# Kernel tuning notes

Measured on AMD Instinct MI355X. Metric: run time of the kernel, lower is better.

Reference implementation:

```python
import jax, jax.numpy as jnp
import numpy as np

D_MODEL = 1024
N_HEAD = 16
D_HEAD = D_MODEL // N_HEAD
B, S = 4, 2048


def setup_inputs() -> dict:
    key = jax.random.key(0)
    ks = jax.random.split(key, 9)
    s = 1.0 / np.sqrt(D_MODEL)
    inp = {"x": jax.random.normal(ks[0], (B, S, D_MODEL), dtype=jnp.float32)}
    for i, name in enumerate(["q", "k", "v", "o"]):
        inp[f"W{name}"] = jax.random.uniform(ks[1 + 2 * i], (D_MODEL, D_MODEL), jnp.float32, -s, s)
        inp[f"b{name}"] = jax.random.uniform(ks[2 + 2 * i], (D_MODEL,), jnp.float32, -s, s)
    return inp


def reference(x, Wq, bq, Wk, bk, Wv, bv, Wo, bo):
    b, sq, _ = x.shape
    skv = sq
    # projections (torch Linear: x @ W^T + b), reshape to (b, h, s, d)
    def proj(W, bias):
        return (x @ W.T + bias).reshape(b, sq, N_HEAD, D_HEAD).transpose(0, 2, 1, 3)
    q, k, v = proj(Wq, bq), proj(Wk, bk), proj(Wv, bv)
    scale = np.sqrt(D_HEAD).astype(np.float32)
    scores = jnp.einsum("bhqd,bhkd->bhqk", q, k) / scale
    causal_mask = jnp.triu(jnp.ones((sq, skv), dtype=bool), k=1)
    scores = jnp.where(causal_mask, -jnp.inf, scores)
    attn = jax.nn.softmax(scores, axis=-1)
    o = jnp.einsum("bhqk,bhkd->bhqd", attn, v)  # (b, h, sq, d_head)
    o = o.transpose(0, 2, 1, 3).reshape(b, sq, D_MODEL)
    return o @ Wo.T + bo
```

## Files before the change

kernel.cpp:

```cpp
#include <hip/hip_runtime.h>
#include <hip/hip_bf16.h>
#include <math.h>

#define S_LEN 2048
#define DMODEL 1024
#define NHEAD 16
#define DHEAD 64
#define BATCH 4
#define MROWS (BATCH * S_LEN)

typedef unsigned short u16;
typedef __attribute__((ext_vector_type(4))) unsigned short u16x4;
typedef __attribute__((ext_vector_type(8))) unsigned short u16x8;
typedef __attribute__((ext_vector_type(2))) unsigned u32x2;
typedef __attribute__((ext_vector_type(4))) unsigned u32x4;
typedef __attribute__((ext_vector_type(8))) short bf16x8;
typedef __attribute__((ext_vector_type(4))) float f32x4;

__device__ __forceinline__ u16 f2bf(float f) {
  unsigned u = __float_as_uint(f);
  u += 0x7fff + ((u >> 16) & 1);
  return (u16)(u >> 16);
}

__device__ __forceinline__ unsigned pkbf2(float lo, float hi) {
  __hip_bfloat162 h = __float22bfloat162_rn(float2{lo, hi});
  unsigned r;
  __builtin_memcpy(&r, &h, 4);
  return r;
}

__device__ __forceinline__ float exp2v(float x) {
  float r;
  asm("v_exp_f32 %0, %1" : "=v"(r) : "v"(x));
  return r;
}

__device__ __forceinline__ f32x4 mfma16(bf16x8 a, bf16x8 b, f32x4 c) {
  return __builtin_amdgcn_mfma_f32_16x16x32_bf16(a, b, c, 0, 0, 0);
}

__global__ __launch_bounds__(256) void castall(
    const float* __restrict__ x,
    const float* __restrict__ w0, const float* __restrict__ w1,
    const float* __restrict__ w2, const float* __restrict__ w3,
    u16* __restrict__ ox,
    u16* __restrict__ o0, u16* __restrict__ o1,
    u16* __restrict__ o2, u16* __restrict__ o3) {
  const int blk = blockIdx.x;
  const float* in;
  u16* out;
  int base;
  if (blk < 4096)      { in = x;  out = ox; base = blk; }
  else if (blk < 4608) { in = w0; out = o0; base = blk - 4096; }
  else if (blk < 5120) { in = w1; out = o1; base = blk - 4608; }
  else if (blk < 5632) { in = w2; out = o2; base = blk - 5120; }
  else                 { in = w3; out = o3; base = blk - 5632; }
  const int i = (base * 256 + threadIdx.x) * 8;
  f32x4 v0 = *(const f32x4*)(in + i);
  f32x4 v1 = *(const f32x4*)(in + i + 4);
  u16x8 o;
#pragma unroll
  for (int j = 0; j < 4; ++j) { o[j] = f2bf(v0[j]); o[4 + j] = f2bf(v1[j]); }
  *(u16x8*)(out + i) = o;
}

__global__ __launch_bounds__(256) void gemm_qkv(
    const u16* __restrict__ Xb,
    const u16* __restrict__ W0, const u16* __restrict__ W1, const u16* __restrict__ W2,
    const float* __restrict__ b0, const float* __restrict__ b1, const float* __restrict__ b2,
    u16* __restrict__ O0, u16* __restrict__ O1, u16* __restrict__ O2) {
  __shared__ u16 As[128 * 64];
  __shared__ u16 Bs[128 * 64];
  const int flat = blockIdx.x;
  const int xcd = flat & 7, idx = flat >> 3;
  const int msub = idx & 7;
  const int nz = idx >> 3;
  const int ymt = xcd * 8 + msub;
  const int xnt = nz & 7;
  const int z = nz >> 3;
  const u16* Wm = z == 0 ? W0 : (z == 1 ? W1 : W2);
  const float* bias = z == 0 ? b0 : (z == 1 ? b1 : b2);
  u16* Out = z == 0 ? O0 : (z == 1 ? O1 : O2);
  const float qs = (z == 0) ? 0.18033688011112042f : 1.0f;
  const int tid = threadIdx.x;
  const int lane = tid & 63, g = lane >> 4, c = lane & 15;
  const int wave = tid >> 6;
  const int wm = wave >> 1, wn = wave & 1;
  const int bm0 = ymt * 128, bn0 = xnt * 128;

  int srow[4], scol[4];
#pragma unroll
  for (int cc = 0; cc < 4; ++cc) {
    const int ci = cc * 256 + tid;
    srow[cc] = ci >> 3;
    scol[cc] = ((ci & 7) ^ (srow[cc] & 7)) << 3;
  }

  f32x4 acc[4][4];
#pragma unroll
  for (int m = 0; m < 4; ++m)
#pragma unroll
    for (int n = 0; n < 4; ++n) acc[m][n] = (f32x4){0.f, 0.f, 0.f, 0.f};

  u32x4 ar0, ar1, ar2, ar3, br0, br1, br2, br3;
#define GLOAD(k0_) do {                                                        \
    ar0 = *(const u32x4*)(Xb + (size_t)(bm0 + srow[0]) * DMODEL + (k0_) + scol[0]); \
    br0 = *(const u32x4*)(Wm + (size_t)(bn0 + srow[0]) * DMODEL + (k0_) + scol[0]); \
    ar1 = *(const u32x4*)(Xb + (size_t)(bm0 + srow[1]) * DMODEL + (k0_) + scol[1]); \
    br1 = *(const u32x4*)(Wm + (size_t)(bn0 + srow[1]) * DMODEL + (k0_) + scol[1]); \
    ar2 = *(const u32x4*)(Xb + (size_t)(bm0 + srow[2]) * DMODEL + (k0_) + scol[2]); \
    br2 = *(const u32x4*)(Wm + (size_t)(bn0 + srow[2]) * DMODEL + (k0_) + scol[2]); \
    ar3 = *(const u32x4*)(Xb + (size_t)(bm0 + srow[3]) * DMODEL + (k0_) + scol[3]); \
    br3 = *(const u32x4*)(Wm + (size_t)(bn0 + srow[3]) * DMODEL + (k0_) + scol[3]); \
  } while (0)

  GLOAD(0);
  for (int k0 = 0; k0 < DMODEL; k0 += 64) {
    __syncthreads();
    *(u32x4*)((char*)As + (0 * 256 + tid) * 16) = ar0;
    *(u32x4*)((char*)Bs + (0 * 256 + tid) * 16) = br0;
    *(u32x4*)((char*)As + (1 * 256 + tid) * 16) = ar1;
    *(u32x4*)((char*)Bs + (1 * 256 + tid) * 16) = br1;
    *(u32x4*)((char*)As + (2 * 256 + tid) * 16) = ar2;
    *(u32x4*)((char*)Bs + (2 * 256 + tid) * 16) = br2;
    *(u32x4*)((char*)As + (3 * 256 + tid) * 16) = ar3;
    *(u32x4*)((char*)Bs + (3 * 256 + tid) * 16) = br3;
    __syncthreads();
    if (k0 + 64 < DMODEL) GLOAD(k0 + 64);
#pragma unroll
    for (int ks = 0; ks < 2; ++ks) {
      bf16x8 af[4], bfr[4];
#pragma unroll
      for (int m = 0; m < 4; ++m) {
        const int arow = wm * 64 + m * 16 + c;
        af[m] = *(const bf16x8*)((const char*)As + arow * 128 +
                                 (((ks * 4 + g) ^ (arow & 7)) << 4));
      }
#pragma unroll
      for (int n = 0; n < 4; ++n) {
        const int brow = wn * 64 + n * 16 + c;
        bfr[n] = *(const bf16x8*)((const char*)Bs + brow * 128 +
                                  (((ks * 4 + g) ^ (brow & 7)) << 4));
      }
#pragma unroll
      for (int m = 0; m < 4; ++m)
#pragma unroll
        for (int n = 0; n < 4; ++n)
          acc[m][n] = mfma16(af[m], bfr[n], acc[m][n]);
    }
  }
#undef GLOAD
  if (z < 2) {
#pragma unroll
    for (int n = 0; n < 4; ++n) {
      const int coln = bn0 + wn * 64 + n * 16 + c;
      const float bn_ = bias[coln];
      const int h = coln >> 6, d = coln & 63;
#pragma unroll
      for (int m = 0; m < 4; ++m) {
#pragma unroll
        for (int r = 0; r < 4; ++r) {
          const int rowm = bm0 + wm * 64 + m * 16 + g * 4 + r;
          const int b_ = rowm >> 11, s_ = rowm & 2047;
          Out[(((size_t)(b_ * NHEAD + h) * S_LEN + s_) << 6) + d] =
              f2bf((acc[m][n][r] + bn_) * qs);
        }
      }
    }
  } else {
#pragma unroll
    for (int n = 0; n < 4; ++n) {
      const int coln = bn0 + wn * 64 + n * 16 + c;
      const float bn_ = bias[coln];
      const int h = coln >> 6, d = coln & 63;
#pragma unroll
      for (int m = 0; m < 4; ++m) {
        const int row0 = bm0 + wm * 64 + m * 16 + g * 4;
        const int b_ = row0 >> 11, s_ = row0 & 2047;
        u16x4 pk;
#pragma unroll
        for (int r = 0; r < 4; ++r) pk[r] = f2bf(acc[m][n][r] + bn_);
        *(u16x4*)(Out + ((size_t)(b_ * NHEAD + h) * DHEAD + d) * S_LEN + s_) = pk;
      }
    }
  }
}

__global__ __launch_bounds__(256) void gemm_out(
    const u16* __restrict__ Ab, const u16* __restrict__ Wm,
    const float* __restrict__ bias, float* __restrict__ Out) {
  __shared__ u16 As[128 * 64];
  __shared__ u16 Bs[128 * 64];
  const int flat = blockIdx.x;
  const int xcd = flat & 7, idx = flat >> 3;
  const int ymt = xcd * 8 + (idx & 7);
  const int xnt = idx >> 3;
  const int tid = threadIdx.x;
  const int lane = tid & 63, g = lane >> 4, c = lane & 15;
  const int wave = tid >> 6;
  const int wm = wave >> 1, wn = wave & 1;
  const int bm0 = ymt * 128, bn0 = xnt * 128;

  int srow[4], scol[4];
#pragma unroll
  for (int cc = 0; cc < 4; ++cc) {
    const int ci = cc * 256 + tid;
    srow[cc] = ci >> 3;
    scol[cc] = ((ci & 7) ^ (srow[cc] & 7)) << 3;
  }

  f32x4 acc[4][4];
#pragma unroll
  for (int m = 0; m < 4; ++m)
#pragma unroll
    for (int n = 0; n < 4; ++n) acc[m][n] = (f32x4){0.f, 0.f, 0.f, 0.f};

  u32x4 ar0, ar1, ar2, ar3, br0, br1, br2, br3;
#define GLOAD(k0_) do {                                                        \
    ar0 = *(const u32x4*)(Ab + (size_t)(bm0 + srow[0]) * DMODEL + (k0_) + scol[0]); \
    br0 = *(const u32x4*)(Wm + (size_t)(bn0 + srow[0]) * DMODEL + (k0_) + scol[0]); \
    ar1 = *(const u32x4*)(Ab + (size_t)(bm0 + srow[1]) * DMODEL + (k0_) + scol[1]); \
    br1 = *(const u32x4*)(Wm + (size_t)(bn0 + srow[1]) * DMODEL + (k0_) + scol[1]); \
    ar2 = *(const u32x4*)(Ab + (size_t)(bm0 + srow[2]) * DMODEL + (k0_) + scol[2]); \
    br2 = *(const u32x4*)(Wm + (size_t)(bn0 + srow[2]) * DMODEL + (k0_) + scol[2]); \
    ar3 = *(const u32x4*)(Ab + (size_t)(bm0 + srow[3]) * DMODEL + (k0_) + scol[3]); \
    br3 = *(const u32x4*)(Wm + (size_t)(bn0 + srow[3]) * DMODEL + (k0_) + scol[3]); \
  } while (0)

  GLOAD(0);
  for (int k0 = 0; k0 < DMODEL; k0 += 64) {
    __syncthreads();
    *(u32x4*)((char*)As + (0 * 256 + tid) * 16) = ar0;
    *(u32x4*)((char*)Bs + (0 * 256 + tid) * 16) = br0;
    *(u32x4*)((char*)As + (1 * 256 + tid) * 16) = ar1;
    *(u32x4*)((char*)Bs + (1 * 256 + tid) * 16) = br1;
    *(u32x4*)((char*)As + (2 * 256 + tid) * 16) = ar2;
    *(u32x4*)((char*)Bs + (2 * 256 + tid) * 16) = br2;
    *(u32x4*)((char*)As + (3 * 256 + tid) * 16) = ar3;
    *(u32x4*)((char*)Bs + (3 * 256 + tid) * 16) = br3;
    __syncthreads();
    if (k0 + 64 < DMODEL) GLOAD(k0 + 64);
#pragma unroll
    for (int ks = 0; ks < 2; ++ks) {
      bf16x8 af[4], bfr[4];
#pragma unroll
      for (int m = 0; m < 4; ++m) {
        const int arow = wm * 64 + m * 16 + c;
        af[m] = *(const bf16x8*)((const char*)As + arow * 128 +
                                 (((ks * 4 + g) ^ (arow & 7)) << 4));
      }
#pragma unroll
      for (int n = 0; n < 4; ++n) {
        const int brow = wn * 64 + n * 16 + c;
        bfr[n] = *(const bf16x8*)((const char*)Bs + brow * 128 +
                                  (((ks * 4 + g) ^ (brow & 7)) << 4));
      }
#pragma unroll
      for (int m = 0; m < 4; ++m)
#pragma unroll
        for (int n = 0; n < 4; ++n)
          acc[m][n] = mfma16(af[m], bfr[n], acc[m][n]);
    }
  }
#undef GLOAD
#pragma unroll
  for (int n = 0; n < 4; ++n) {
    const int coln = bn0 + wn * 64 + n * 16 + c;
    const float bn_ = bias[coln];
#pragma unroll
    for (int m = 0; m < 4; ++m) {
#pragma unroll
      for (int r = 0; r < 4; ++r) {
        const int rowm = bm0 + wm * 64 + m * 16 + g * 4 + r;
        Out[(size_t)rowm * DMODEL + coln] = acc[m][n][r] + bn_;
      }
    }
  }
}

__global__ __launch_bounds__(512) void attn_fwd(const u16* __restrict__ Qb,
                                                const u16* __restrict__ Kb,
                                                const u16* __restrict__ VTb,
                                                u16* __restrict__ AOb) {
  __shared__ u16 Kt[64 * 64];
  __shared__ u16 Vt[64 * 64];
  __shared__ unsigned Pl[8][16 * 36];
  const int tid = threadIdx.x;
  const int w = tid >> 6, lane = tid & 63, g = lane >> 4, c = lane & 15;
  const int flat = blockIdx.x;
  const int xcd = flat & 7, idx = flat >> 3;
  const int qt16 = 15 - (idx >> 3);
  const int bh = xcd * 8 + (idx & 7);
  const size_t base = (size_t)bh * (S_LEN * DHEAD);
  const int b_ = bh >> 4, h = bh & 15;

  const int row0_ = tid >> 3, colg0 = (tid & 7) ^ (row0_ & 7);

  const int qb = qt16 * 128;
  const int q = qb + w * 16 + c;
  const bf16x8 qf0 = *(const bf16x8*)(Qb + base + (size_t)q * 64 + g * 8);
  const bf16x8 qf1 = *(const bf16x8*)(Qb + base + (size_t)q * 64 + 32 + g * 8);

  bf16x8 ones;
#pragma unroll
  for (int j = 0; j < 8; ++j) ones[j] = (short)0x3F80;

  f32x4 oacc[4];
  f32x4 lacc = (f32x4){0.f, 0.f, 0.f, 0.f};
#pragma unroll
  for (int dt = 0; dt < 4; ++dt) oacc[dt] = (f32x4){0.f, 0.f, 0.f, 0.f};
  float m = -30000.f;

  u32x4 kreg0, vreg0;
#define STAGE_LOAD(kt_) do {                                                  \
    const int kv0_ = (kt_) * 64;                                              \
    kreg0 = *(const u32x4*)(Kb + base + (size_t)(kv0_ + row0_) * 64 + colg0 * 8); \
    vreg0 = *(const u32x4*)(VTb + base + (size_t)row0_ * S_LEN + kv0_ + colg0 * 8); \
  } while (0)

  const int nt = 2 * qt16 + 2;
  STAGE_LOAD(0);
  for (int kt = 0; kt < nt; ++kt) {
    const int kv0 = kt * 64;
    __syncthreads();
    *(u32x4*)((char*)Kt + tid * 16) = kreg0;
    *(u32x4*)((char*)Vt + tid * 16) = vreg0;
    __syncthreads();
    if (kt + 1 < nt) STAGE_LOAD(kt + 1);

    f32x4 s[4];
#pragma unroll
    for (int t = 0; t < 4; ++t) {
      const int krow = t * 16 + c;
      const char* kbase = (const char*)Kt + krow * 128;
      bf16x8 kf0 = *(const bf16x8*)(kbase + ((g ^ (krow & 7)) * 16));
      bf16x8 kf1 = *(const bf16x8*)(kbase + (((4 + g) ^ (krow & 7)) * 16));
      f32x4 zacc = (f32x4){0.f, 0.f, 0.f, 0.f};
      zacc = mfma16(kf0, qf0, zacc);
      zacc = mfma16(kf1, qf1, zacc);
      s[t] = zacc;
    }
    if (kt >= nt - 2) {
#pragma unroll
      for (int t = 0; t < 4; ++t)
#pragma unroll
        for (int r = 0; r < 4; ++r)
          if (kv0 + t * 16 + 4 * g + r > q) s[t][r] = -30000.f;
    }
    const float a0 = fmaxf(fmaxf(s[0][0], s[0][1]), s[0][2]);
    const float a1 = fmaxf(fmaxf(s[0][3], s[1][0]), s[1][1]);
    const float a2 = fmaxf(fmaxf(s[1][2], s[1][3]), s[2][0]);
    const float a3 = fmaxf(fmaxf(s[2][1], s[2][2]), s[2][3]);
    const float a4 = fmaxf(fmaxf(s[3][0], s[3][1]), s[3][2]);
    float pm = fmaxf(fmaxf(fmaxf(a0, a1), a2), fmaxf(fmaxf(a3, a4), s[3][3]));
    pm = fmaxf(pm, __shfl_xor(pm, 16));
    pm = fmaxf(pm, __shfl_xor(pm, 32));
    if (__any(pm > m + 8.0f)) {
      const float mn = fmaxf(m, pm);
      const float sc = exp2v(m - mn);
      lacc *= sc;
#pragma unroll
      for (int dt = 0; dt < 4; ++dt) oacc[dt] *= sc;
      m = mn;
    }
#pragma unroll
    for (int t = 0; t < 4; ++t) {
      const float p0 = exp2v(s[t][0] - m), p1 = exp2v(s[t][1] - m);
      const float p2 = exp2v(s[t][2] - m), p3 = exp2v(s[t][3] - m);
      u32x2 pk2;
      pk2[0] = pkbf2(p0, p1);
      pk2[1] = pkbf2(p2, p3);
      *(u32x2*)&Pl[w][c * 36 + t * 8 + g * 2] = pk2;
    }

#pragma unroll
    for (int kk = 0; kk < 2; ++kk) {
      const bf16x8 pb = *(const bf16x8*)&Pl[w][c * 36 + kk * 16 + g * 4];
      lacc = mfma16(ones, pb, lacc);
#pragma unroll
      for (int dt = 0; dt < 4; ++dt) {
        const int vrow = dt * 16 + c;
        const bf16x8 vf = *(const bf16x8*)((const char*)Vt + vrow * 128 +
                                           (((kk * 4 + g) ^ (vrow & 7)) * 16));
        oacc[dt] = mfma16(vf, pb, oacc[dt]);
      }
    }
  }
#undef STAGE_LOAD
  const float inv = 1.0f / lacc[0];
  const size_t rowbase = ((size_t)(b_ * S_LEN + q) * DMODEL) + h * 64;
#pragma unroll
  for (int dt = 0; dt < 4; ++dt) {
    u16x4 pk4;
#pragma unroll
    for (int r = 0; r < 4; ++r) pk4[r] = f2bf(oacc[dt][r] * inv);
    *(u16x4*)(AOb + rowbase + dt * 16 + 4 * g) = pk4;
  }
}

extern "C" void kernel_launch(void* const* d_in, const int* in_sizes, int n_in,
                              void* d_out, int out_size, void* d_ws, size_t ws_size,
                              hipStream_t stream) {
  const float* x  = (const float*)d_in[0];
  const float* Wq = (const float*)d_in[1];
  const float* bq = (const float*)d_in[2];
  const float* Wk = (const float*)d_in[3];
  const float* bk = (const float*)d_in[4];
  const float* Wv = (const float*)d_in[5];
  const float* bv = (const float*)d_in[6];
  const float* Wo = (const float*)d_in[7];
  const float* bo = (const float*)d_in[8];
  float* out = (float*)d_out;
  char* ws = (char*)d_ws;

  const size_t MB = 1024 * 1024;
  u16* xb  = (u16*)(ws);
  u16* Wqb = (u16*)(ws + 16 * MB);
  u16* Wkb = (u16*)(ws + 18 * MB);
  u16* Wvb = (u16*)(ws + 20 * MB);
  u16* Wob = (u16*)(ws + 22 * MB);
  u16* Qb  = (u16*)(ws + 24 * MB);
  u16* Kb  = (u16*)(ws + 40 * MB);
  u16* VTb = (u16*)(ws + 56 * MB);
  u16* AOb = (u16*)(ws + 72 * MB);

  castall<<<6144, 256, 0, stream>>>(x, Wq, Wk, Wv, Wo, xb, Wqb, Wkb, Wvb, Wob);

  gemm_qkv<<<1536, 256, 0, stream>>>(
      xb, Wqb, Wkb, Wvb, bq, bk, bv, Qb, Kb, VTb);

  attn_fwd<<<1024, 512, 0, stream>>>(Qb, Kb, VTb, AOb);

  gemm_out<<<512, 256, 0, stream>>>(AOb, Wob, bo, out);
}
```

Measured before the change: 158.3 us.

## Enlarge QKV GEMM tile to 256x128 with 512-thread blocks

Doubles the M dimension of the QKV projection GEMM block tile to 256 rows and uses 8 waves per block, so each staged B (weight) tile is reused across twice as many rows. Grid is halved to 768 blocks and LDS for A doubles. The aim is to cut global and LDS traffic per FLOP, at the cost of fewer blocks, higher LDS use per block and possibly lower occupancy.

```diff
diff --git a/kernel.cpp b/kernel.cpp
--- a/kernel.cpp
+++ b/kernel.cpp
@@ -65,18 +65,18 @@
   *(u16x8*)(out + i) = o;
 }
 
-__global__ __launch_bounds__(256) void gemm_qkv(
+__global__ __launch_bounds__(512) void gemm_qkv(
     const u16* __restrict__ Xb,
     const u16* __restrict__ W0, const u16* __restrict__ W1, const u16* __restrict__ W2,
     const float* __restrict__ b0, const float* __restrict__ b1, const float* __restrict__ b2,
     u16* __restrict__ O0, u16* __restrict__ O1, u16* __restrict__ O2) {
-  __shared__ u16 As[128 * 64];
+  __shared__ u16 As[256 * 64];
   __shared__ u16 Bs[128 * 64];
   const int flat = blockIdx.x;
   const int xcd = flat & 7, idx = flat >> 3;
-  const int msub = idx & 7;
-  const int nz = idx >> 3;
-  const int ymt = xcd * 8 + msub;
+  const int msub = idx & 3;
+  const int nz = idx >> 2;
+  const int ymt = xcd * 4 + msub;
   const int xnt = nz & 7;
   const int z = nz >> 3;
   const u16* Wm = z == 0 ? W0 : (z == 1 ? W1 : W2);
@@ -87,14 +87,20 @@
   const int lane = tid & 63, g = lane >> 4, c = lane & 15;
   const int wave = tid >> 6;
   const int wm = wave >> 1, wn = wave & 1;
-  const int bm0 = ymt * 128, bn0 = xnt * 128;
-
-  int srow[4], scol[4];
+  const int bm0 = ymt * 256, bn0 = xnt * 128;
+
+  int arowS[4], acolS[4], browS[2], bcolS[2];
 #pragma unroll
   for (int cc = 0; cc < 4; ++cc) {
-    const int ci = cc * 256 + tid;
-    srow[cc] = ci >> 3;
-    scol[cc] = ((ci & 7) ^ (srow[cc] & 7)) << 3;
+    const int ci = cc * 512 + tid;
+    arowS[cc] = ci >> 3;
+    acolS[cc] = ((ci & 7) ^ (arowS[cc] & 7)) << 3;
+  }
+#pragma unroll
+  for (int cc = 0; cc < 2; ++cc) {
+    const int ci = cc * 512 + tid;
+    browS[cc] = ci >> 3;
+    bcolS[cc] = ((ci & 7) ^ (browS[cc] & 7)) << 3;
   }
 
   f32x4 acc[4][4];
@@ -103,29 +109,25 @@
 #pragma unroll
     for (int n = 0; n < 4; ++n) acc[m][n] = (f32x4){0.f, 0.f, 0.f, 0.f};
 
-  u32x4 ar0, ar1, ar2, ar3, br0, br1, br2, br3;
+  u32x4 ar0, ar1, ar2, ar3, br0, br1;
 #define GLOAD(k0_) do {                                                        \
-    ar0 = *(const u32x4*)(Xb + (size_t)(bm0 + srow[0]) * DMODEL + (k0_) + scol[0]); \
-    br0 = *(const u32x4*)(Wm + (size_t)(bn0 + srow[0]) * DMODEL + (k0_) + scol[0]); \
-    ar1 = *(const u32x4*)(Xb + (size_t)(bm0 + srow[1]) * DMODEL + (k0_) + scol[1]); \
-    br1 = *(const u32x4*)(Wm + (size_t)(bn0 + srow[1]) * DMODEL + (k0_) + scol[1]); \
-    ar2 = *(const u32x4*)(Xb + (size_t)(bm0 + srow[2]) * DMODEL + (k0_) + scol[2]); \
-    br2 = *(const u32x4*)(Wm + (size_t)(bn0 + srow[2]) * DMODEL + (k0_) + scol[2]); \
-    ar3 = *(const u32x4*)(Xb + (size_t)(bm0 + srow[3]) * DMODEL + (k0_) + scol[3]); \
-    br3 = *(const u32x4*)(Wm + (size_t)(bn0 + srow[3]) * DMODEL + (k0_) + scol[3]); \
+    ar0 = *(const u32x4*)(Xb + (size_t)(bm0 + arowS[0]) * DMODEL + (k0_) + acolS[0]); \
+    ar1 = *(const u32x4*)(Xb + (size_t)(bm0 + arowS[1]) * DMODEL + (k0_) + acolS[1]); \
+    ar2 = *(const u32x4*)(Xb + (size_t)(bm0 + arowS[2]) * DMODEL + (k0_) + acolS[2]); \
+    ar3 = *(const u32x4*)(Xb + (size_t)(bm0 + arowS[3]) * DMODEL + (k0_) + acolS[3]); \
+    br0 = *(const u32x4*)(Wm + (size_t)(bn0 + browS[0]) * DMODEL + (k0_) + bcolS[0]); \
+    br1 = *(const u32x4*)(Wm + (size_t)(bn0 + browS[1]) * DMODEL + (k0_) + bcolS[1]); \
   } while (0)
 
   GLOAD(0);
   for (int k0 = 0; k0 < DMODEL; k0 += 64) {
     __syncthreads();
-    *(u32x4*)((char*)As + (0 * 256 + tid) * 16) = ar0;
-    *(u32x4*)((char*)Bs + (0 * 256 + tid) * 16) = br0;
-    *(u32x4*)((char*)As + (1 * 256 + tid) * 16) = ar1;
-    *(u32x4*)((char*)Bs + (1 * 256 + tid) * 16) = br1;
-    *(u32x4*)((char*)As + (2 * 256 + tid) * 16) = ar2;
-    *(u32x4*)((char*)Bs + (2 * 256 + tid) * 16) = br2;
-    *(u32x4*)((char*)As + (3 * 256 + tid) * 16) = ar3;
-    *(u32x4*)((char*)Bs + (3 * 256 + tid) * 16) = br3;
+    *(u32x4*)((char*)As + (0 * 512 + tid) * 16) = ar0;
+    *(u32x4*)((char*)As + (1 * 512 + tid) * 16) = ar1;
+    *(u32x4*)((char*)As + (2 * 512 + tid) * 16) = ar2;
+    *(u32x4*)((char*)As + (3 * 512 + tid) * 16) = ar3;
+    *(u32x4*)((char*)Bs + (0 * 512 + tid) * 16) = br0;
+    *(u32x4*)((char*)Bs + (1 * 512 + tid) * 16) = br1;
     __syncthreads();
     if (k0 + 64 < DMODEL) GLOAD(k0 + 64);
 #pragma unroll
@@ -427,7 +429,7 @@
 
   castall<<<6144, 256, 0, stream>>>(x, Wq, Wk, Wv, Wo, xb, Wqb, Wkb, Wvb, Wob);
 
-  gemm_qkv<<<1536, 256, 0, stream>>>(
+  gemm_qkv<<<768, 512, 0, stream>>>(
       xb, Wqb, Wkb, Wvb, bq, bk, bv, Qb, Kb, VTb);
 
   attn_fwd<<<1024, 512, 0, stream>>>(Qb, Kb, VTb, AOb);
```

New measurement: 158.1 us. No clear change (-0.1%).
